# Kernel optimization log

Measured on AMD Instinct MI355X. Metric: run time of the kernel, lower is better.

The kernel has to match this reference:

```python
import jax, jax.numpy as jnp
import numpy as np

B, D, K, P = 512, 2048, 128, 5

def setup_inputs() -> dict:
    key = jax.random.key(0)
    k1, k2 = jax.random.split(key)
    x = jax.random.normal(k1, (B, D), dtype=jnp.float32)
    theta = 0.05 * jax.random.normal(k2, (D, K, P), dtype=jnp.float32)
    log_weight_scale = jnp.zeros((K, P), dtype=jnp.float32)
    bias = -jnp.ones((K,), dtype=jnp.float32)  # layer inits bias to -1
    return {"x": x, "theta": theta, "log_weight_scale": log_weight_scale, "bias": bias}

def reference(x, theta, log_weight_scale, bias):
    b = x.shape[0]
    # weight-normalized kernel: [D, K, P]
    norm = jnp.sqrt(jnp.sum(theta * theta, axis=0))            # [K, P]
    kernel = theta * (jnp.exp(log_weight_scale) / norm)[None]  # [D, K, P]
    actv = jnp.einsum('bd,dkp->bkp', x, kernel)                # [B, K, P]
    # pairwise L1 over P: [B, K, B]
    diff = jnp.abs(actv[:, :, :, None] - jnp.transpose(actv, (1, 2, 0))[None])  # [B,K,P,B]
    abs_dif = jnp.sum(diff, axis=2) + 1e6 * jnp.eye(b, dtype=x.dtype)[:, None, :]
    f = jnp.sum(jnp.exp(-abs_dif), axis=2) + bias[None, :]     # [B, K]
    return jnp.concatenate([x, f], axis=1)                     # [B, D+K]
```

## Files before the change

kernel.cpp:

```cpp
#include <hip/hip_runtime.h>
#include <math.h>

#define BSZ 512
#define DD 2048
#define KK 128
#define PP 5
#define NCOL (KK * PP)
#define OUTW (DD + KK)
#define LOG2E 1.4426950408889634f

#define KSPLIT 16
#define GK (DD / KSPLIT)
#define QSPLIT 8

typedef __attribute__((ext_vector_type(8))) short bf16x8;
typedef __attribute__((ext_vector_type(4))) float f32x4;

#define WS_NORM 0
#define WS_ACTV (WS_NORM + NCOL)
#define WS_FPART (WS_ACTV + BSZ * NCOL)
#define WS_XB (WS_FPART + QSPLIT * KK * BSZ)
#define WS_THT (WS_XB + BSZ * DD / 2)
#define WS_PART (WS_THT + NCOL * DD / 2)

__device__ inline ushort f2b(float f) {
    unsigned u = __float_as_uint(f);
    u += 0x7FFF + ((u >> 16) & 1);
    return (ushort)(u >> 16);
}

#define SWZ(r, c) ((((r) * 128) + ((c) ^ (((r) & 7) << 3))))

__global__ __launch_bounds__(256) void prep_kernel(const float* __restrict__ theta,
                                                   const float* __restrict__ x,
                                                   float* __restrict__ norm,
                                                   ushort* __restrict__ thT,
                                                   ushort* __restrict__ xb) {
    __shared__ float partial[32][8];
    __shared__ ushort sT[64][68];

    const int bid = blockIdx.x;
    const int t   = threadIdx.x;

    if (bid < 80) {
        const int c8  = bid * 8;
        const int col = c8 + (t & 7);
        const int g   = t >> 3;
        const float* p = theta + (size_t)g * NCOL + col;
        float s = 0.f;
#pragma unroll
        for (int j = 0; j < 64; ++j) {
            float v = p[(size_t)j * 32 * NCOL];
            s += v * v;
        }
        partial[g][t & 7] = s;
        __syncthreads();
        if (t < 8) {
            float acc = 0.f;
#pragma unroll
            for (int gg = 0; gg < 32; ++gg) acc += partial[gg][t];
            norm[c8 + t] = acc;
        }
    } else if (bid < 400) {
        const int tb    = bid - 80;
        const int kz    = (tb & 31) * 64;
        const int nz    = (tb >> 5) * 64;
        const int c4    = t & 15;
        const int rbase = t >> 4;
#pragma unroll
        for (int i = 0; i < 4; ++i) {
            int r = rbase + i * 16;
            float4 v = *(const float4*)&theta[(size_t)(kz + r) * NCOL + nz + c4 * 4];
            sT[c4 * 4 + 0][r] = f2b(v.x);
            sT[c4 * 4 + 1][r] = f2b(v.y);
            sT[c4 * 4 + 2][r] = f2b(v.z);
            sT[c4 * 4 + 3][r] = f2b(v.w);
        }
        __syncthreads();
#pragma unroll
        for (int i = 0; i < 2; ++i) {
            int slot = t + i * 256;
            int rr   = slot >> 3;
            int cc   = (slot & 7) * 8;
            ushort4 w0 = *(const ushort4*)&sT[rr][cc];
            ushort4 w1 = *(const ushort4*)&sT[rr][cc + 4];
            ushort* dst = &thT[(size_t)(nz + rr) * DD + kz + cc];
            *(ushort4*)&dst[0] = w0;
            *(ushort4*)&dst[4] = w1;
        }
    } else {
        const int b2 = bid - 400;
#pragma unroll
        for (int i = 0; i < 4; ++i) {
            int base = b2 * 4096 + i * 1024 + t * 4;
            float4 v = *(const float4*)&x[base];
            ushort4 w;
            w.x = f2b(v.x); w.y = f2b(v.y); w.z = f2b(v.z); w.w = f2b(v.w);
            *(ushort4*)&xb[base] = w;
        }
    }
}

__global__ __launch_bounds__(256) void gemm_kernel(const ushort* __restrict__ xb,
                                                   const ushort* __restrict__ thT,
                                                   float* __restrict__ part,
                                                   const float* __restrict__ x,
                                                   float* __restrict__ out) {
    __shared__ ushort lA[64 * 128];
    __shared__ ushort lB[64 * 128];

    const int bx = blockIdx.x;
    if (bx >= 1280) {
        const int bid = bx - 1280;
        for (int i = bid * 256 + threadIdx.x; i < BSZ * (DD / 4); i += 80 * 256) {
            int r = i >> 9;
            int c = i & 511;
            float4 v = *(const float4*)&x[(size_t)r * DD + c * 4];
            *(float4*)&out[(size_t)r * OUTW + c * 4] = v;
        }
        return;
    }

    const int t    = threadIdx.x;
    const int lane = t & 63;
    const int wave = t >> 6;
    const int tile = bx % 80;
    const int z    = bx / 80;
    const int bn   = (tile % 10) * 64;
    const int bm   = (tile / 10) * 64;
    const int kz   = z * GK;

    const ushort* gA = xb  + (size_t)bm * DD + kz;
    const ushort* gB = thT + (size_t)bn * DD + kz;

    const int srr = t >> 4;
    const int sss = t & 15;

    uint4 va[4], vb[4];
#pragma unroll
    for (int i = 0; i < 4; ++i) {
        int rr = srr + i * 16;
        va[i] = *(const uint4*)&gA[(size_t)rr * DD + sss * 8];
        vb[i] = *(const uint4*)&gB[(size_t)rr * DD + sss * 8];
    }
#pragma unroll
    for (int i = 0; i < 4; ++i) {
        int rr = srr + i * 16;
        *(uint4*)&lA[SWZ(rr, sss * 8)] = va[i];
        *(uint4*)&lB[SWZ(rr, sss * 8)] = vb[i];
    }
    __syncthreads();

    const int fr = lane & 15;
    const int g  = lane >> 4;
    const int mr = (wave >> 1) * 32 + fr;
    const int nr = (wave & 1) * 32 + fr;

    f32x4 acc[2][2] = {};
#pragma unroll
    for (int ks = 0; ks < 4; ++ks) {
        const int kc = ks * 32 + g * 8;
        bf16x8 a0 = *(const bf16x8*)&lA[SWZ(mr,      kc)];
        bf16x8 a1 = *(const bf16x8*)&lA[SWZ(mr + 16, kc)];
        bf16x8 b0 = *(const bf16x8*)&lB[SWZ(nr,      kc)];
        bf16x8 b1 = *(const bf16x8*)&lB[SWZ(nr + 16, kc)];
        acc[0][0] = __builtin_amdgcn_mfma_f32_16x16x32_bf16(a0, b0, acc[0][0], 0, 0, 0);
        acc[0][1] = __builtin_amdgcn_mfma_f32_16x16x32_bf16(a0, b1, acc[0][1], 0, 0, 0);
        acc[1][0] = __builtin_amdgcn_mfma_f32_16x16x32_bf16(a1, b0, acc[1][0], 0, 0, 0);
        acc[1][1] = __builtin_amdgcn_mfma_f32_16x16x32_bf16(a1, b1, acc[1][1], 0, 0, 0);
    }

    float* base = part + (size_t)z * (BSZ * NCOL);
#pragma unroll
    for (int mt = 0; mt < 2; ++mt)
#pragma unroll
        for (int nt = 0; nt < 2; ++nt) {
            int row = bm + (wave >> 1) * 32 + mt * 16 + g * 4;
            int col = bn + (wave & 1) * 32 + nt * 16 + fr;
            float* dst = base + (size_t)row * NCOL + col;
#pragma unroll
            for (int reg = 0; reg < 4; ++reg)
                dst[(size_t)reg * NCOL] = acc[mt][nt][reg];
        }
}

__global__ __launch_bounds__(256) void reduce_kernel(const float* __restrict__ part,
                                                     const float* __restrict__ norm,
                                                     const float* __restrict__ lws,
                                                     float* __restrict__ actv) {
    int i   = blockIdx.x * 256 + threadIdx.x;
    int col = i % NCOL;
    float s = 0.f;
#pragma unroll
    for (int q = 0; q < KSPLIT; ++q)
        s += part[(size_t)q * (BSZ * NCOL) + i];
    const float scale = __builtin_amdgcn_exp2f(lws[col] * LOG2E) *
                        __builtin_amdgcn_rsqf(norm[col]) * LOG2E;
    actv[i] = s * scale;
}

__global__ __launch_bounds__(256) void pairwise_kernel(const float* __restrict__ actv,
                                                       float* __restrict__ f_part) {
    const int k   = blockIdx.x;
    const int q   = blockIdx.y;
    const int tid = threadIdx.x;

    __shared__ float sB[64][8];

    for (int i = tid; i < 64 * PP; i += 256) {
        int r = i / PP;
        int p = i - r * PP;
        sB[r][p] = actv[(size_t)(q * 64 + r) * NCOL + k * PP + p];
    }

    float a[2][PP];
#pragma unroll
    for (int r = 0; r < 2; ++r) {
        const float* ap = &actv[(size_t)(tid + r * 256) * NCOL + k * PP];
#pragma unroll
        for (int p = 0; p < PP; ++p) a[r][p] = ap[p];
    }
    __syncthreads();

    float acc[2] = {0.f, 0.f};
#pragma unroll 4
    for (int j = 0; j < 64; ++j) {
        const float4 v  = *(const float4*)&sB[j][0];
        const float  v4 = sB[j][4];
#pragma unroll
        for (int r = 0; r < 2; ++r) {
            float s = fabsf(a[r][0] - v.x) + fabsf(a[r][1] - v.y) +
                      fabsf(a[r][2] - v.z) + fabsf(a[r][3] - v.w) +
                      fabsf(a[r][4] - v4);
            acc[r] += __builtin_amdgcn_exp2f(-s);
        }
    }

    float* fp = f_part + ((size_t)q * KK + k) * BSZ;
    fp[tid]       = acc[0];
    fp[tid + 256] = acc[1];
}

__global__ __launch_bounds__(256) void freduce_kernel(const float* __restrict__ f_part,
                                                      const float* __restrict__ bias,
                                                      float* __restrict__ out) {
    int i = blockIdx.x * 256 + threadIdx.x;
    int k = i >> 9;
    int b = i & 511;
    float s = 0.f;
#pragma unroll
    for (int q = 0; q < QSPLIT; ++q)
        s += f_part[((size_t)q * KK + k) * BSZ + b];
    out[(size_t)b * OUTW + DD + k] = s - 1.0f + bias[k];
}

extern "C" void kernel_launch(void* const* d_in, const int* in_sizes, int n_in,
                              void* d_out, int out_size, void* d_ws, size_t ws_size,
                              hipStream_t stream) {
    const float* x     = (const float*)d_in[0];
    const float* theta = (const float*)d_in[1];
    const float* lws   = (const float*)d_in[2];
    const float* bias  = (const float*)d_in[3];
    float* out = (float*)d_out;

    float* ws     = (float*)d_ws;
    float* norm   = ws + WS_NORM;
    float* actv   = ws + WS_ACTV;
    float* f_part = ws + WS_FPART;
    ushort* xb    = (ushort*)(ws + WS_XB);
    ushort* thT   = (ushort*)(ws + WS_THT);
    float* part   = ws + WS_PART;

    prep_kernel<<<656, 256, 0, stream>>>(theta, x, norm, thT, xb);
    gemm_kernel<<<1360, 256, 0, stream>>>(xb, thT, part, x, out);
    reduce_kernel<<<(BSZ * NCOL) / 256, 256, 0, stream>>>(part, norm, lws, actv);
    pairwise_kernel<<<dim3(KK, QSPLIT), 256, 0, stream>>>(actv, f_part);
    freduce_kernel<<<256, 256, 0, stream>>>(f_part, bias, out);
}
```

Baseline: 104.0 us.

## Store split-K GEMM partials as bf16, vectorize reduce, read pairwise operands via scalar loads

The GEMM now writes its split-K partial sums as bf16 instead of fp32, which halves the partial-buffer write and read traffic. The reduce kernel handles two columns per thread with packed loads and a float2 store. Block indexing is remapped so adjacent blocks share the same N tile and K slice. The pairwise kernel drops its LDS staging and __syncthreads and reads the broadcast operands through a wave-uniform pointer, so they can become scalar loads. Rounding partials to bf16 before summing adds error to the activations, and that error goes through the exponential in the pairwise step.

```diff
diff --git a/kernel.cpp b/kernel.cpp
--- a/kernel.cpp
+++ b/kernel.cpp
@@ -103,7 +103,7 @@
 
 __global__ __launch_bounds__(256) void gemm_kernel(const ushort* __restrict__ xb,
                                                    const ushort* __restrict__ thT,
-                                                   float* __restrict__ part,
+                                                   ushort* __restrict__ parth,
                                                    const float* __restrict__ x,
                                                    float* __restrict__ out) {
     __shared__ ushort lA[64 * 128];
@@ -124,10 +124,11 @@
     const int t    = threadIdx.x;
     const int lane = t & 63;
     const int wave = t >> 6;
-    const int tile = bx % 80;
-    const int z    = bx / 80;
-    const int bn   = (tile % 10) * 64;
-    const int bm   = (tile / 10) * 64;
+    const int mt8  = bx & 7;
+    const int rest = bx >> 3;
+    const int bn   = (rest % 10) * 64;
+    const int bm   = mt8 * 64;
+    const int z    = rest / 10;
     const int kz   = z * GK;
 
     const ushort* gA = xb  + (size_t)bm * DD + kz;
@@ -170,33 +171,39 @@
         acc[1][1] = __builtin_amdgcn_mfma_f32_16x16x32_bf16(a1, b1, acc[1][1], 0, 0, 0);
     }
 
-    float* base = part + (size_t)z * (BSZ * NCOL);
+    ushort* base = parth + (size_t)z * (BSZ * NCOL);
 #pragma unroll
     for (int mt = 0; mt < 2; ++mt)
 #pragma unroll
         for (int nt = 0; nt < 2; ++nt) {
             int row = bm + (wave >> 1) * 32 + mt * 16 + g * 4;
             int col = bn + (wave & 1) * 32 + nt * 16 + fr;
-            float* dst = base + (size_t)row * NCOL + col;
+            ushort* dst = base + (size_t)row * NCOL + col;
 #pragma unroll
             for (int reg = 0; reg < 4; ++reg)
-                dst[(size_t)reg * NCOL] = acc[mt][nt][reg];
-        }
-}
-
-__global__ __launch_bounds__(256) void reduce_kernel(const float* __restrict__ part,
+                dst[(size_t)reg * NCOL] = f2b(acc[mt][nt][reg]);
+        }
+}
+
+__global__ __launch_bounds__(256) void reduce_kernel(const ushort* __restrict__ parth,
                                                      const float* __restrict__ norm,
                                                      const float* __restrict__ lws,
                                                      float* __restrict__ actv) {
-    int i   = blockIdx.x * 256 + threadIdx.x;
-    int col = i % NCOL;
-    float s = 0.f;
-#pragma unroll
-    for (int q = 0; q < KSPLIT; ++q)
-        s += part[(size_t)q * (BSZ * NCOL) + i];
-    const float scale = __builtin_amdgcn_exp2f(lws[col] * LOG2E) *
-                        __builtin_amdgcn_rsqf(norm[col]) * LOG2E;
-    actv[i] = s * scale;
+    int i = (blockIdx.x * 256 + threadIdx.x) * 2;
+    float s0 = 0.f, s1 = 0.f;
+#pragma unroll
+    for (int q = 0; q < KSPLIT; ++q) {
+        unsigned u = *(const unsigned*)&parth[(size_t)q * (BSZ * NCOL) + i];
+        s0 += __uint_as_float(u << 16);
+        s1 += __uint_as_float(u & 0xffff0000u);
+    }
+    const int col = i % NCOL;
+    const float sc0 = __builtin_amdgcn_exp2f(lws[col] * LOG2E) *
+                      __builtin_amdgcn_rsqf(norm[col]) * LOG2E;
+    const float sc1 = __builtin_amdgcn_exp2f(lws[col + 1] * LOG2E) *
+                      __builtin_amdgcn_rsqf(norm[col + 1]) * LOG2E;
+    float2 o = make_float2(s0 * sc0, s1 * sc1);
+    *(float2*)&actv[i] = o;
 }
 
 __global__ __launch_bounds__(256) void pairwise_kernel(const float* __restrict__ actv,
@@ -205,14 +212,6 @@
     const int q   = blockIdx.y;
     const int tid = threadIdx.x;
 
-    __shared__ float sB[64][8];
-
-    for (int i = tid; i < 64 * PP; i += 256) {
-        int r = i / PP;
-        int p = i - r * PP;
-        sB[r][p] = actv[(size_t)(q * 64 + r) * NCOL + k * PP + p];
-    }
-
     float a[2][PP];
 #pragma unroll
     for (int r = 0; r < 2; ++r) {
@@ -220,17 +219,22 @@
 #pragma unroll
         for (int p = 0; p < PP; ++p) a[r][p] = ap[p];
     }
-    __syncthreads();
+
+    const int ubase = __builtin_amdgcn_readfirstlane(q * 64 * NCOL + k * PP);
+    const float* __restrict__ up = actv + ubase;
 
     float acc[2] = {0.f, 0.f};
-#pragma unroll 4
+#pragma unroll 8
     for (int j = 0; j < 64; ++j) {
-        const float4 v  = *(const float4*)&sB[j][0];
-        const float  v4 = sB[j][4];
+        const float v0 = up[j * NCOL + 0];
+        const float v1 = up[j * NCOL + 1];
+        const float v2 = up[j * NCOL + 2];
+        const float v3 = up[j * NCOL + 3];
+        const float v4 = up[j * NCOL + 4];
 #pragma unroll
         for (int r = 0; r < 2; ++r) {
-            float s = fabsf(a[r][0] - v.x) + fabsf(a[r][1] - v.y) +
-                      fabsf(a[r][2] - v.z) + fabsf(a[r][3] - v.w) +
+            float s = fabsf(a[r][0] - v0) + fabsf(a[r][1] - v1) +
+                      fabsf(a[r][2] - v2) + fabsf(a[r][3] - v3) +
                       fabsf(a[r][4] - v4);
             acc[r] += __builtin_amdgcn_exp2f(-s);
         }
@@ -269,11 +273,11 @@
     float* f_part = ws + WS_FPART;
     ushort* xb    = (ushort*)(ws + WS_XB);
     ushort* thT   = (ushort*)(ws + WS_THT);
-    float* part   = ws + WS_PART;
+    ushort* parth = (ushort*)(ws + WS_PART);
 
     prep_kernel<<<656, 256, 0, stream>>>(theta, x, norm, thT, xb);
-    gemm_kernel<<<1360, 256, 0, stream>>>(xb, thT, part, x, out);
-    reduce_kernel<<<(BSZ * NCOL) / 256, 256, 0, stream>>>(part, norm, lws, actv);
+    gemm_kernel<<<1360, 256, 0, stream>>>(xb, thT, parth, x, out);
+    reduce_kernel<<<640, 256, 0, stream>>>(parth, norm, lws, actv);
     pairwise_kernel<<<dim3(KK, QSPLIT), 256, 0, stream>>>(actv, f_part);
     freduce_kernel<<<256, 256, 0, stream>>>(f_part, bias, out);
 }
```

Measured after the change: 101.5 us. 1.03x faster.
